# Kernel tuning notes

Measured on AMD Instinct MI355X. Metric: run time of the kernel, lower is better.

## Reference

```python
import jax, jax.numpy as jnp
import numpy as np

N = 10000   # num_nodes (= input feature dim, identity-style features)
E = 320000  # edges (avg degree 32)
P = 200000  # candidate node pairs
H1, H2 = 32, 16


def gcn_conv(x, W, b, edge_index, num_nodes):
    # PyG GCNConv: add self-loops, symmetric D^-1/2 (A+I) D^-1/2 normalization,
    # linear transform, scatter-add aggregation, then bias.
    loop = jnp.arange(num_nodes)
    src = jnp.concatenate([edge_index[0], loop])
    dst = jnp.concatenate([edge_index[1], loop])
    deg = jax.ops.segment_sum(jnp.ones_like(src, dtype=x.dtype), dst,
                              num_segments=num_nodes)  # includes self-loop, so deg >= 1
    dinv = jax.lax.rsqrt(deg)
    norm = dinv[src] * dinv[dst]                       # [E+N]
    h = x @ W                                          # [N, out]
    out = jax.ops.segment_sum(h[src] * norm[:, None], dst, num_segments=num_nodes)
    return out + b


def setup_inputs() -> dict:
    key = jax.random.key(0)
    ks = jax.random.split(key, 9)
    x = jax.random.normal(ks[0], (N, N), dtype=jnp.float32)
    edge_index = jax.random.randint(ks[1], (2, E), 0, N)
    pair_index = jax.random.randint(ks[2], (P, 2), 0, N)
    W1 = jax.random.normal(ks[3], (N, H1), dtype=jnp.float32) * 0.01
    b1 = jnp.zeros((H1,), jnp.float32)
    W2 = jax.random.normal(ks[4], (H1, H2), dtype=jnp.float32) * 0.1
    b2 = jnp.zeros((H2,), jnp.float32)
    Wfc = jax.random.normal(ks[5], (2 * H2, 1), dtype=jnp.float32) * 0.1
    bfc = jnp.zeros((1,), jnp.float32)
    return {"x": x, "edge_index": edge_index, "pair_index": pair_index,
            "W1": W1, "b1": b1, "W2": W2, "b2": b2, "Wfc": Wfc, "bfc": bfc}


def reference(x, edge_index, pair_index, W1, b1, W2, b2, Wfc, bfc):
    h = jax.nn.relu(gcn_conv(x, W1, b1, edge_index, N))   # [N, 32]
    h = gcn_conv(h, W2, b2, edge_index, N)                # [N, 16]
    pair = jnp.concatenate([h[pair_index[:, 0]], h[pair_index[:, 1]]], axis=1)  # [P, 32]
    return jax.nn.sigmoid(pair @ Wfc + bfc)               # [P, 1]
```

## Files before the change

### kernel.cpp

```cpp
#include <hip/hip_runtime.h>
#include <hip/hip_fp16.h>
#include <math.h>

#define NN 10000
#define EE 320000
#define PP 200000
#define NTILES 320
#define KSPL 1024
#define NSPL 10

typedef _Float16 h8v __attribute__((ext_vector_type(8)));
typedef __attribute__((ext_vector_type(4))) float f4v;

#define GLOAD_LDS16(gsrc, ldst)                                                        \
    __builtin_amdgcn_global_load_lds((const __attribute__((address_space(1))) void*)(gsrc), \
                                     (__attribute__((address_space(3))) void*)(ldst), 16, 0, 0)

__device__ __forceinline__ ushort f2h(float f) {
    union { _Float16 h; ushort u; } c;
    c.h = (_Float16)f;
    return c.u;
}

__global__ void k_deg_count(const int* __restrict__ dst, int* __restrict__ degi) {
    int e = blockIdx.x * blockDim.x + threadIdx.x;
    if (e < EE) atomicAdd(&degi[dst[e]], 1);
}

__global__ void k_dinv(const int* __restrict__ degi, float* __restrict__ dinv) {
    int n = blockIdx.x * blockDim.x + threadIdx.x;
    if (n < NN) dinv[n] = rsqrtf((float)(degi[n] + 1));
}

__global__ void k_wprep(const float* __restrict__ W1, ushort* __restrict__ wf) {
    int t = blockIdx.x * blockDim.x + threadIdx.x;
    if (t >= NTILES * 2 * 64 * 8) return;
    int e = t & 7, lane = (t >> 3) & 63, ct = (t >> 9) & 1, g = t >> 10;
    int col = ct * 16 + (lane & 15);
    int k = g * 32 + (lane >> 4) * 8 + e;
    wf[t] = (k < NN) ? f2h(W1[(long)k * 32 + col]) : (ushort)0;
}

__global__ __launch_bounds__(64) void k_gemm1(const float* __restrict__ x,
                                              const ushort* __restrict__ w1f,
                                              const float* __restrict__ zp,
                                              float* __restrict__ h1_part) {
    __shared__ __align__(16) float xs[16][260];
    const int lane = threadIdx.x;
    const int fl = lane & 15;
    const int khi = lane >> 4;
    const int ks = blockIdx.y;
    const int wrow0 = blockIdx.x * 16;
    const long NN2 = (long)NN * NN;

    f4v acc0 = (f4v){0.f, 0.f, 0.f, 0.f};
    f4v acc1 = (f4v){0.f, 0.f, 0.f, 0.f};

#pragma unroll
    for (int half = 0; half < 4; ++half) {
        const int kbase = ks * KSPL + half * 256;
        const int gbase8 = ks * 32 + half * 8;

#pragma unroll
        for (int j = 0; j < 16; ++j) {
            long flat = (long)(wrow0 + j) * NN + kbase + lane * 4;
            const float* src = (flat + 4 <= NN2) ? (x + flat) : zp;
            GLOAD_LDS16(src, &xs[j][0]);
        }
        h8v wr[8][2];
#pragma unroll
        for (int kk = 0; kk < 8; ++kk)
#pragma unroll
            for (int ct = 0; ct < 2; ++ct)
                wr[kk][ct] = *(const h8v*)(w1f + ((long)((gbase8 + kk) * 2 + ct) * 64 + lane) * 8);

        asm volatile("s_waitcnt vmcnt(0)" ::: "memory");
        __builtin_amdgcn_sched_barrier(0);

#pragma unroll
        for (int kk = 0; kk < 8; ++kk) {
            const float4* ap = (const float4*)&xs[fl][kk * 32 + khi * 8];
            float4 f0 = ap[0];
            float4 f1 = ap[1];
            union { h8v v; _Float16 h[8]; } a;
            a.h[0] = (_Float16)f0.x; a.h[1] = (_Float16)f0.y;
            a.h[2] = (_Float16)f0.z; a.h[3] = (_Float16)f0.w;
            a.h[4] = (_Float16)f1.x; a.h[5] = (_Float16)f1.y;
            a.h[6] = (_Float16)f1.z; a.h[7] = (_Float16)f1.w;
            acc0 = __builtin_amdgcn_mfma_f32_16x16x32_f16(a.v, wr[kk][0], acc0, 0, 0, 0);
            acc1 = __builtin_amdgcn_mfma_f32_16x16x32_f16(a.v, wr[kk][1], acc1, 0, 0, 0);
        }
        asm volatile("s_waitcnt lgkmcnt(0)" ::: "memory");
        __builtin_amdgcn_sched_barrier(0);
    }

    const long pbase = (long)ks * NN * 32;
#pragma unroll
    for (int ct = 0; ct < 2; ++ct) {
        f4v a = ct ? acc1 : acc0;
        const int col = ct * 16 + fl;
#pragma unroll
        for (int r = 0; r < 4; ++r) {
            int g = wrow0 + khi * 4 + r;
            h1_part[pbase + (long)g * 32 + col] = a[r];
        }
    }
}

__global__ void k_selfinit1(const float4* __restrict__ h1_part4, const float* __restrict__ dinv,
                            float4* __restrict__ h1_pre4, __half* __restrict__ out1h) {
    int t = blockIdx.x * blockDim.x + threadIdx.x;
    if (t >= NN * 8) return;
    float4 s = make_float4(0.f, 0.f, 0.f, 0.f);
#pragma unroll
    for (int ks = 0; ks < NSPL; ++ks) {
        float4 v = h1_part4[(long)ks * NN * 8 + t];
        s.x += v.x; s.y += v.y; s.z += v.z; s.w += v.w;
    }
    int n = t >> 3;
    float d2 = dinv[n] * dinv[n];
    h1_pre4[t] = s;
    __half2 lo = __floats2half2_rn(s.x * d2, s.y * d2);
    __half2 hi = __floats2half2_rn(s.z * d2, s.w * d2);
    union { struct { __half2 a, b; } h; uint2 u; } p;
    p.h.a = lo; p.h.b = hi;
    *(uint2*)(out1h + (long)t * 4) = p.u;
}

__global__ void k_scatter1(const int* __restrict__ src, const int* __restrict__ dst,
                           const float* __restrict__ dinv, const float* __restrict__ h1_pre,
                           __half2* __restrict__ out1h2) {
    int t = blockIdx.x * blockDim.x + threadIdx.x;
    if (t >= EE * 16) return;
    int e = t >> 4, p = t & 15;
    int s = src[e], d = dst[e];
    float nrm = dinv[s] * dinv[d];
    const float2 hv = *(const float2*)&h1_pre[s * 32 + p * 2];
    __half2 val = __floats2half2_rn(hv.x * nrm, hv.y * nrm);
    unsafeAtomicAdd(&out1h2[d * 16 + p], val);
}

__global__ __launch_bounds__(256) void k_gemm2(const __half* __restrict__ out1h,
                                               const float* __restrict__ W2,
                                               const float* __restrict__ b1,
                                               const float* __restrict__ dinv,
                                               float* __restrict__ h2_pre,
                                               __half* __restrict__ out2h) {
    __shared__ float w2s[512];
    __shared__ float b1s[32];
    int tid = threadIdx.x;
    w2s[tid] = W2[tid & 511];
    if (tid < 256) w2s[256 + tid] = W2[256 + tid];
    if (tid < 32) b1s[tid] = b1[tid];
    __syncthreads();
    int c = tid & 15, yloc = tid >> 4;
    int n = blockIdx.x * 16 + yloc;
    if (n < NN) {
        float a = 0.f;
#pragma unroll
        for (int k = 0; k < 32; ++k) {
            float v = fmaxf(__half2float(out1h[n * 32 + k]) + b1s[k], 0.f);
            a += v * w2s[k * 16 + c];
        }
        h2_pre[n * 16 + c] = a;
        float di = dinv[n];
        out2h[n * 16 + c] = __float2half(di * di * a);
    }
}

__global__ void k_scatter2(const int* __restrict__ src, const int* __restrict__ dst,
                           const float* __restrict__ dinv, const float* __restrict__ h2_pre,
                           __half2* __restrict__ out2h2) {
    int t = blockIdx.x * blockDim.x + threadIdx.x;
    if (t >= EE * 8) return;
    int e = t >> 3, p = t & 7;
    int s = src[e], d = dst[e];
    float nrm = dinv[s] * dinv[d];
    const float2 hv = *(const float2*)&h2_pre[s * 16 + p * 2];
    __half2 val = __floats2half2_rn(hv.x * nrm, hv.y * nrm);
    unsafeAtomicAdd(&out2h2[d * 8 + p], val);
}

__global__ void k_final2(const __half* __restrict__ out2h, const float* __restrict__ b2,
                         const float* __restrict__ Wfc, float* __restrict__ s_arr,
                         float* __restrict__ t_arr) {
    int n = blockIdx.x * blockDim.x + threadIdx.x;
    if (n >= NN) return;
    float s = 0.f, t = 0.f;
#pragma unroll
    for (int c = 0; c < 16; ++c) {
        float v = __half2float(out2h[n * 16 + c]) + b2[c];
        s += v * Wfc[c];
        t += v * Wfc[16 + c];
    }
    s_arr[n] = s;
    t_arr[n] = t;
}

__global__ void k_pairs(const int* __restrict__ pair, const float* __restrict__ s_arr,
                        const float* __restrict__ t_arr, const float* __restrict__ bfc,
                        float* __restrict__ out) {
    int p = blockIdx.x * blockDim.x + threadIdx.x;
    if (p >= PP) return;
    const int2 ab = ((const int2*)pair)[p];
    float z = s_arr[ab.x] + t_arr[ab.y] + bfc[0];
    out[p] = 1.f / (1.f + expf(-z));
}

extern "C" void kernel_launch(void* const* d_in, const int* in_sizes, int n_in,
                              void* d_out, int out_size, void* d_ws, size_t ws_size,
                              hipStream_t stream) {
    const float* x    = (const float*)d_in[0];
    const int*   edge = (const int*)d_in[1];
    const int*   pair = (const int*)d_in[2];
    const float* W1   = (const float*)d_in[3];
    const float* b1   = (const float*)d_in[4];
    const float* W2   = (const float*)d_in[5];
    const float* b2   = (const float*)d_in[6];
    const float* Wfc  = (const float*)d_in[7];
    const float* bfc  = (const float*)d_in[8];
    float* out = (float*)d_out;
    float* ws  = (float*)d_ws;

    const int* src = edge;
    const int* dst = edge + EE;

    int*    degi    = (int*)ws;
    float*  dinv    = ws + NN;
    float*  h1_pre  = ws + 2 * NN;
    __half* out1h   = (__half*)(ws + 34 * NN);
    float*  h2_pre  = ws + 66 * NN;
    __half* out2h   = (__half*)(ws + 82 * NN);
    float*  s_arr   = ws + 98 * NN;
    float*  t_arr   = ws + 99 * NN;
    float*  zp      = ws + 100 * NN;
    ushort* w1f     = (ushort*)(ws + 100 * NN + 256);
    float*  h1_part = ws + 100 * NN + 256 + 163840;

    hipMemsetAsync(degi, 0, NN * sizeof(int), stream);
    hipMemsetAsync(zp, 0, 1024, stream);

    k_deg_count<<<(EE + 255) / 256, 256, 0, stream>>>(dst, degi);
    k_dinv<<<(NN + 255) / 256, 256, 0, stream>>>(degi, dinv);
    k_wprep<<<(NTILES * 2 * 64 * 8 + 255) / 256, 256, 0, stream>>>(W1, w1f);

    k_gemm1<<<dim3(625, NSPL), 64, 0, stream>>>(x, w1f, zp, h1_part);

    k_selfinit1<<<(NN * 8 + 255) / 256, 256, 0, stream>>>(
        (const float4*)h1_part, dinv, (float4*)h1_pre, out1h);

    k_scatter1<<<(EE * 16 + 255) / 256, 256, 0, stream>>>(src, dst, dinv, h1_pre,
                                                          (__half2*)out1h);

    k_gemm2<<<(NN + 15) / 16, 256, 0, stream>>>(out1h, W2, b1, dinv, h2_pre, out2h);

    k_scatter2<<<(EE * 8 + 255) / 256, 256, 0, stream>>>(src, dst, dinv, h2_pre,
                                                         (__half2*)out2h);

    k_final2<<<(NN + 255) / 256, 256, 0, stream>>>(out2h, b2, Wfc, s_arr, t_arr);
    k_pairs<<<(PP + 255) / 256, 256, 0, stream>>>(pair, s_arr, t_arr, bfc, out);
}
```

Measured before the change: 175.9 us.

## Double-buffer x tiles in GEMM1 and fold memsets into weight-prep kernel

The GEMM1 kernel now keeps two LDS buffers, so the global-to-LDS load of the next 256-wide K chunk overlaps the MFMA compute on the current one, and it preloads all W1 fragments for the four chunks up front. Separately, the two hipMemsetAsync calls are replaced by zeroing degi and the zero pad inside k_wprep, which now runs first, removing two launches. The trade-off is more LDS and many more VGPRs held for the 64 W fragments, which could hurt occupancy or cause spills.

```diff
diff --git a/kernel.cpp b/kernel.cpp
--- a/kernel.cpp
+++ b/kernel.cpp
@@ -32,8 +32,11 @@
     if (n < NN) dinv[n] = rsqrtf((float)(degi[n] + 1));
 }
 
-__global__ void k_wprep(const float* __restrict__ W1, ushort* __restrict__ wf) {
-    int t = blockIdx.x * blockDim.x + threadIdx.x;
+__global__ void k_wprep(const float* __restrict__ W1, ushort* __restrict__ wf,
+                        int* __restrict__ degi, float* __restrict__ zp) {
+    int t = blockIdx.x * blockDim.x + threadIdx.x;
+    if (t < NN) degi[t] = 0;
+    if (t < 256) zp[t] = 0.f;
     if (t >= NTILES * 2 * 64 * 8) return;
     int e = t & 7, lane = (t >> 3) & 63, ct = (t >> 9) & 1, g = t >> 10;
     int col = ct * 16 + (lane & 15);
@@ -45,7 +48,7 @@
                                               const ushort* __restrict__ w1f,
                                               const float* __restrict__ zp,
                                               float* __restrict__ h1_part) {
-    __shared__ __align__(16) float xs[16][260];
+    __shared__ __align__(16) float xs[2][16][260];
     const int lane = threadIdx.x;
     const int fl = lane & 15;
     const int khi = lane >> 4;
@@ -53,33 +56,33 @@
     const int wrow0 = blockIdx.x * 16;
     const long NN2 = (long)NN * NN;
 
-    f4v acc0 = (f4v){0.f, 0.f, 0.f, 0.f};
-    f4v acc1 = (f4v){0.f, 0.f, 0.f, 0.f};
-
-#pragma unroll
-    for (int half = 0; half < 4; ++half) {
-        const int kbase = ks * KSPL + half * 256;
-        const int gbase8 = ks * 32 + half * 8;
-
+    h8v wr[4][8][2];
+#pragma unroll
+    for (int c = 0; c < 4; ++c)
+#pragma unroll
+        for (int kk = 0; kk < 8; ++kk)
+#pragma unroll
+            for (int ct = 0; ct < 2; ++ct)
+                wr[c][kk][ct] = *(const h8v*)(w1f +
+                    ((long)((ks * 32 + c * 8 + kk) * 2 + ct) * 64 + lane) * 8);
+
+    auto stage = [&](int buf, int c) {
+        const int kbase = ks * KSPL + c * 256;
 #pragma unroll
         for (int j = 0; j < 16; ++j) {
             long flat = (long)(wrow0 + j) * NN + kbase + lane * 4;
             const float* src = (flat + 4 <= NN2) ? (x + flat) : zp;
-            GLOAD_LDS16(src, &xs[j][0]);
-        }
-        h8v wr[8][2];
-#pragma unroll
-        for (int kk = 0; kk < 8; ++kk)
-#pragma unroll
-            for (int ct = 0; ct < 2; ++ct)
-                wr[kk][ct] = *(const h8v*)(w1f + ((long)((gbase8 + kk) * 2 + ct) * 64 + lane) * 8);
-
-        asm volatile("s_waitcnt vmcnt(0)" ::: "memory");
-        __builtin_amdgcn_sched_barrier(0);
-
+            GLOAD_LDS16(src, &xs[buf][j][0]);
+        }
+    };
+
+    f4v acc0 = (f4v){0.f, 0.f, 0.f, 0.f};
+    f4v acc1 = (f4v){0.f, 0.f, 0.f, 0.f};
+
+    auto compute = [&](int buf, int c) {
 #pragma unroll
         for (int kk = 0; kk < 8; ++kk) {
-            const float4* ap = (const float4*)&xs[fl][kk * 32 + khi * 8];
+            const float4* ap = (const float4*)&xs[buf][fl][kk * 32 + khi * 8];
             float4 f0 = ap[0];
             float4 f1 = ap[1];
             union { h8v v; _Float16 h[8]; } a;
@@ -87,12 +90,23 @@
             a.h[2] = (_Float16)f0.z; a.h[3] = (_Float16)f0.w;
             a.h[4] = (_Float16)f1.x; a.h[5] = (_Float16)f1.y;
             a.h[6] = (_Float16)f1.z; a.h[7] = (_Float16)f1.w;
-            acc0 = __builtin_amdgcn_mfma_f32_16x16x32_f16(a.v, wr[kk][0], acc0, 0, 0, 0);
-            acc1 = __builtin_amdgcn_mfma_f32_16x16x32_f16(a.v, wr[kk][1], acc1, 0, 0, 0);
-        }
-        asm volatile("s_waitcnt lgkmcnt(0)" ::: "memory");
-        __builtin_amdgcn_sched_barrier(0);
-    }
+            acc0 = __builtin_amdgcn_mfma_f32_16x16x32_f16(a.v, wr[c][kk][0], acc0, 0, 0, 0);
+            acc1 = __builtin_amdgcn_mfma_f32_16x16x32_f16(a.v, wr[c][kk][1], acc1, 0, 0, 0);
+        }
+    };
+
+    stage(0, 0);
+    stage(1, 1);
+
+#define WAITV(n) asm volatile("s_waitcnt vmcnt(" #n ")" ::: "memory"); __builtin_amdgcn_sched_barrier(0)
+#define WAITL()  asm volatile("s_waitcnt lgkmcnt(0)" ::: "memory");    __builtin_amdgcn_sched_barrier(0)
+
+    WAITV(16); compute(0, 0); WAITL(); stage(0, 2);
+    WAITV(16); compute(1, 1); WAITL(); stage(1, 3);
+    WAITV(16); compute(0, 2);
+    WAITV(0);  compute(1, 3);
+#undef WAITV
+#undef WAITL
 
     const long pbase = (long)ks * NN * 32;
 #pragma unroll
@@ -237,12 +251,9 @@
     ushort* w1f     = (ushort*)(ws + 100 * NN + 256);
     float*  h1_part = ws + 100 * NN + 256 + 163840;
 
-    hipMemsetAsync(degi, 0, NN * sizeof(int), stream);
-    hipMemsetAsync(zp, 0, 1024, stream);
-
+    k_wprep<<<(NTILES * 2 * 64 * 8 + 255) / 256, 256, 0, stream>>>(W1, w1f, degi, zp);
     k_deg_count<<<(EE + 255) / 256, 256, 0, stream>>>(dst, degi);
     k_dinv<<<(NN + 255) / 256, 256, 0, stream>>>(degi, dinv);
-    k_wprep<<<(NTILES * 2 * 64 * 8 + 255) / 256, 256, 0, stream>>>(W1, w1f);
 
     k_gemm1<<<dim3(625, NSPL), 64, 0, stream>>>(x, w1f, zp, h1_part);
 
```

Measured after the change: 179.0 us. No clear change (+1.7%).
